# Optimization experiments

Hardware: AMD Instinct MI355X
Metric: run time of the kernel (lower is better)

Reference implementation:

```python
import jax, jax.numpy as jnp
import numpy as np

B, T, DIN, DOUT = 64, 512, 512, 512


def setup_inputs() -> dict:
    key = jax.random.key(0)
    ks = jax.random.split(key, 16)
    s = 0.05  # small scale ~ xavier/orthogonal magnitude
    inp = {
        "X": jax.random.normal(ks[0], (B, T, DIN), jnp.float32),
        "Wi": jax.random.normal(ks[1], (DOUT, DIN), jnp.float32) * s,
        "bi": jnp.zeros((DOUT,), jnp.float32),
        "Wf": jax.random.normal(ks[2], (DOUT, DIN), jnp.float32) * s,
        "bf": jnp.ones((DOUT,), jnp.float32),
        "Wc": jax.random.normal(ks[3], (DOUT, DIN), jnp.float32) * s,
        "bc": jnp.zeros((DOUT,), jnp.float32),
        "Wo": jax.random.normal(ks[4], (DOUT, DIN), jnp.float32) * s,
        "bo": jnp.zeros((DOUT,), jnp.float32),
        "Ui": jax.random.normal(ks[5], (DOUT, DOUT), jnp.float32) * s,
        "Uf": jax.random.normal(ks[6], (DOUT, DOUT), jnp.float32) * s,
        "bUf": jax.random.normal(ks[7], (DOUT,), jnp.float32) * s,
        "Uc": jax.random.normal(ks[8], (DOUT, DOUT), jnp.float32) * s,
        "bUc": jax.random.normal(ks[9], (DOUT,), jnp.float32) * s,
        "Uo": jax.random.normal(ks[10], (DOUT, DOUT), jnp.float32) * s,
        "bUo": jax.random.normal(ks[11], (DOUT,), jnp.float32) * s,
    }
    return inp


def reference(X, Wi, bi, Wf, bf, Wc, bc, Wo, bo, Ui, Uf, bUf, Uc, bUc, Uo, bUo):
    # Inference mode: dropout masks are ones, initial h/c are zeros.
    # Precompute input projections for all timesteps (as in the original).
    Xi = jnp.einsum('btd,od->bto', X, Wi) + bi  # [B,T,DOUT]
    Xf = jnp.einsum('btd,od->bto', X, Wf) + bf  # computed but UNUSED (faithful to source bug)
    Xc = jnp.einsum('btd,od->bto', X, Wc) + bc
    Xo = jnp.einsum('btd,od->bto', X, Wo) + bo

    h0 = jnp.zeros((X.shape[0], Wi.shape[0]), X.dtype)
    c0 = jnp.zeros_like(h0)

    def step(carry, xs):
        h, c = carry
        xi, xc, xo = xs
        i = jax.nn.sigmoid(xi + h @ Ui.T)                 # U_i has no bias
        f = jax.nn.sigmoid(xi + h @ Uf.T + bUf)           # NOTE: uses xi, not xf (source quirk)
        c_new = f * c + i * jnp.tanh(xc + h @ Uc.T + bUc)
        o = jax.nn.sigmoid(xo + h @ Uo.T + bUo)
        h_new = o * jnp.tanh(c_new)
        return (h_new, c_new), (h_new, c_new)

    xs = (Xi.transpose(1, 0, 2), Xc.transpose(1, 0, 2), Xo.transpose(1, 0, 2))  # [T,B,D]
    _, (H, C) = jax.lax.scan(step, (h0, c0), xs)
    return H.transpose(1, 0, 2), C.transpose(1, 0, 2)  # [B,T,DOUT] each
```

## Files before the change

### kernel.cpp

```cpp
#include <hip/hip_runtime.h>

#define B_    64
#define T_    512
#define D_    512
#define KF    1024
#define NGRP  4
#define NSLC  16
#define GB    16

using short8 = __attribute__((ext_vector_type(8))) short;
using f32x4  = __attribute__((ext_vector_type(4))) float;

__device__ __forceinline__ unsigned short f2bf(float f) {
    unsigned int u = __float_as_uint(f);
    u = (u + 0x7fffu + ((u >> 16) & 1u)) >> 16;
    return (unsigned short)u;
}
__device__ __forceinline__ float sigmf(float x)  { return 1.0f / (1.0f + __expf(-x)); }
__device__ __forceinline__ float tanh_f(float x) { return 1.0f - 2.0f / (1.0f + __expf(2.0f * x)); }

__global__ void prep_x(const float* __restrict__ X, unsigned short* __restrict__ Xb, int n4) {
    int stride = gridDim.x * blockDim.x;
    for (int i = blockIdx.x * blockDim.x + threadIdx.x; i < n4; i += stride) {
        float4 v = ((const float4*)X)[i];
        ushort4 o;
        o.x = f2bf(v.x); o.y = f2bf(v.y); o.z = f2bf(v.z); o.w = f2bf(v.w);
        ((ushort4*)Xb)[i] = o;
    }
}

__global__ void prep_w(const float* __restrict__ Wi, const float* __restrict__ Wc,
                       const float* __restrict__ Wo,
                       const float* __restrict__ Ui, const float* __restrict__ Uf,
                       const float* __restrict__ Uc, const float* __restrict__ Uo,
                       unsigned short* __restrict__ Wcat) {
    int idx = blockIdx.x * blockDim.x + threadIdx.x;
    if (idx >= 2048 * 1024) return;
    int r = idx >> 10, k = idx & 1023;
    int o = r >> 2, g = r & 3;
    const float* U = (g == 0) ? Ui : (g == 1) ? Uf : (g == 2) ? Uc : Uo;
    const float* W = (g < 2) ? Wi : (g == 2) ? Wc : Wo;
    float v = (k < 512) ? U[o * 512 + k] : W[o * 512 + (k - 512)];
    Wcat[idx] = f2bf(v);
}

__attribute__((amdgpu_waves_per_eu(2, 2)))
__launch_bounds__(512)
__global__ void lstm_rec(const unsigned short* __restrict__ Xb,
                         const unsigned short* __restrict__ Wcat,
                         unsigned short* __restrict__ hbuf,
                         unsigned int* __restrict__ hflag,
                         float* __restrict__ out,
                         const float* __restrict__ bi, const float* __restrict__ bc,
                         const float* __restrict__ bo, const float* __restrict__ bUf,
                         const float* __restrict__ bUc, const float* __restrict__ bUo) {
    __shared__ unsigned char Hl[16 * 1024];
    __shared__ unsigned char Xl[16 * 1024];

    const int tid  = threadIdx.x;
    const int bid  = blockIdx.x;
    const int g    = bid >> 4;
    const int s    = bid & 15;
    const int wave = tid >> 6;
    const int lane = tid & 63;
    const int q    = lane >> 4;
    const int bl   = lane & 15;

    const unsigned short* wrow = Wcat + (size_t)(s * 128 + wave * 16 + bl) * KF + q * 8;
    short8 Uh[16], Ux[16];
    #pragma unroll
    for (int kt = 0; kt < 16; ++kt) {
        union { unsigned long long u[2]; short8 v; } wh, wx;
        const unsigned long long* ph = (const unsigned long long*)(wrow + kt * 32);
        const unsigned long long* px = (const unsigned long long*)(wrow + 512 + kt * 32);
        wh.u[0] = __hip_atomic_load(ph,     __ATOMIC_RELAXED, __HIP_MEMORY_SCOPE_AGENT);
        wh.u[1] = __hip_atomic_load(ph + 1, __ATOMIC_RELAXED, __HIP_MEMORY_SCOPE_AGENT);
        wx.u[0] = __hip_atomic_load(px,     __ATOMIC_RELAXED, __HIP_MEMORY_SCOPE_AGENT);
        wx.u[1] = __hip_atomic_load(px + 1, __ATOMIC_RELAXED, __HIP_MEMORY_SCOPE_AGENT);
        Uh[kt] = wh.v;
        Ux[kt] = wx.v;
    }

    const int og = s * 32 + wave * 4 + q;
    const float bi0 = bi[og],           bf0 = bi[og] + bUf[og];
    const float bc0 = bc[og] + bUc[og], bo0 = bo[og] + bUo[og];
    float cst = 0.f;

    const int sb  = tid >> 5;
    const int seg = tid & 31;
    const int sx  = (sb & 7) << 4;
    unsigned int* pollp = hflag + (size_t)(g * NSLC + (seg >> 1)) * 16;
    unsigned int* myfl  = hflag + (size_t)(g * NSLC + s) * 16;
    const unsigned short* xst = Xb + (size_t)(g * GB + sb) * T_ * D_ + seg * 16;

    const unsigned short* xbl = Xb + (size_t)(g * GB + bl) * T_ * D_ + q * 8;
    const int abase = bl * 1024;
    const int axor  = (bl & 7) << 4;
    const int kq16  = q * 16;

    float* Hout = out;
    float* Cout = out + (size_t)B_ * T_ * D_;

    f32x4 xa0 = {0.f, 0.f, 0.f, 0.f}, xa1 = {0.f, 0.f, 0.f, 0.f};
    #pragma unroll
    for (int kt = 0; kt < 16; kt += 2) {
        short8 b0 = *(const short8*)(xbl + kt * 32);
        short8 b1 = *(const short8*)(xbl + (kt + 1) * 32);
        xa0 = __builtin_amdgcn_mfma_f32_16x16x32_bf16(Ux[kt],     b0, xa0, 0, 0, 0);
        xa1 = __builtin_amdgcn_mfma_f32_16x16x32_bf16(Ux[kt + 1], b1, xa1, 0, 0, 0);
    }

    for (int t = 0; t < T_; ++t) {
        uint4 xr0, xr1;
        const bool hasNext = (t + 1 < T_);
        if (hasNext) {
            const uint4* xs = (const uint4*)(xst + (size_t)(t + 1) * D_);
            xr0 = xs[0]; xr1 = xs[1];
        }

        f32x4 ha0 = {0.f, 0.f, 0.f, 0.f}, ha1 = {0.f, 0.f, 0.f, 0.f};
        if (t > 0) {
            while (__hip_atomic_load(pollp, __ATOMIC_RELAXED, __HIP_MEMORY_SCOPE_AGENT) < (unsigned)t) { }
            asm volatile("" ::: "memory");
            const unsigned long long* hs = (const unsigned long long*)
                (hbuf + ((size_t)((t + 1) & 1) * B_ + g * GB + sb) * D_ + seg * 16);
            unsigned long long d0 = __hip_atomic_load(hs + 0, __ATOMIC_RELAXED, __HIP_MEMORY_SCOPE_AGENT);
            unsigned long long d1 = __hip_atomic_load(hs + 1, __ATOMIC_RELAXED, __HIP_MEMORY_SCOPE_AGENT);
            unsigned long long d2 = __hip_atomic_load(hs + 2, __ATOMIC_RELAXED, __HIP_MEMORY_SCOPE_AGENT);
            unsigned long long d3 = __hip_atomic_load(hs + 3, __ATOMIC_RELAXED, __HIP_MEMORY_SCOPE_AGENT);
            *(uint4*)(Hl + sb * 1024 + ((seg * 32)      ^ sx)) =
                make_uint4((unsigned)d0, (unsigned)(d0 >> 32), (unsigned)d1, (unsigned)(d1 >> 32));
            *(uint4*)(Hl + sb * 1024 + ((seg * 32 + 16) ^ sx)) =
                make_uint4((unsigned)d2, (unsigned)(d2 >> 32), (unsigned)d3, (unsigned)(d3 >> 32));
            __syncthreads();
            #pragma unroll
            for (int kt = 0; kt < 16; kt += 2) {
                short8 a0 = *(const short8*)(Hl + abase + ((kq16 + kt * 64)       ^ axor));
                short8 a1 = *(const short8*)(Hl + abase + ((kq16 + (kt + 1) * 64) ^ axor));
                ha0 = __builtin_amdgcn_mfma_f32_16x16x32_bf16(Uh[kt],     a0, ha0, 0, 0, 0);
                ha1 = __builtin_amdgcn_mfma_f32_16x16x32_bf16(Uh[kt + 1], a1, ha1, 0, 0, 0);
            }
        }

        if (hasNext) {
            *(uint4*)(Xl + sb * 1024 + ((seg * 32)      ^ sx)) = xr0;
            *(uint4*)(Xl + sb * 1024 + ((seg * 32 + 16) ^ sx)) = xr1;
        }

        f32x4 A = (ha0 + ha1) + (xa0 + xa1);
        float iv = sigmf(A[0] + bi0);
        float fv = sigmf(A[1] + bf0);
        float cc = tanh_f(A[2] + bc0);
        float ov = sigmf(A[3] + bo0);
        float cv = fv * cst + iv * cc;
        float hv = ov * tanh_f(cv);
        cst = cv;

        __hip_atomic_store(hbuf + ((size_t)(t & 1) * B_ + g * GB + bl) * D_ + og,
                           f2bf(hv), __ATOMIC_RELAXED, __HIP_MEMORY_SCOPE_AGENT);
        __syncthreads();
        if (tid == 0)
            __hip_atomic_store(myfl, (unsigned)(t + 1), __ATOMIC_RELAXED, __HIP_MEMORY_SCOPE_AGENT);

        if (hasNext) {
            f32x4 n0 = {0.f, 0.f, 0.f, 0.f}, n1 = {0.f, 0.f, 0.f, 0.f};
            #pragma unroll
            for (int kt = 0; kt < 16; kt += 2) {
                short8 b0 = *(const short8*)(Xl + abase + ((kq16 + kt * 64)       ^ axor));
                short8 b1 = *(const short8*)(Xl + abase + ((kq16 + (kt + 1) * 64) ^ axor));
                n0 = __builtin_amdgcn_mfma_f32_16x16x32_bf16(Ux[kt],     b0, n0, 0, 0, 0);
                n1 = __builtin_amdgcn_mfma_f32_16x16x32_bf16(Ux[kt + 1], b1, n1, 0, 0, 0);
            }
            xa0 = n0; xa1 = n1;
        }

        const size_t oi = ((size_t)(g * GB + bl) * T_ + t) * D_ + og;
        Hout[oi] = hv;
        Cout[oi] = cv;
    }
}

extern "C" void kernel_launch(void* const* d_in, const int* in_sizes, int n_in,
                              void* d_out, int out_size, void* d_ws, size_t ws_size,
                              hipStream_t stream) {
    const float* X   = (const float*)d_in[0];
    const float* Wi  = (const float*)d_in[1];
    const float* bi  = (const float*)d_in[2];
    const float* Wc  = (const float*)d_in[5];
    const float* bc  = (const float*)d_in[6];
    const float* Wo  = (const float*)d_in[7];
    const float* bo  = (const float*)d_in[8];
    const float* Ui  = (const float*)d_in[9];
    const float* Uf  = (const float*)d_in[10];
    const float* bUf = (const float*)d_in[11];
    const float* Uc  = (const float*)d_in[12];
    const float* bUc = (const float*)d_in[13];
    const float* Uo  = (const float*)d_in[14];
    const float* bUo = (const float*)d_in[15];

    char* ws = (char*)d_ws;
    const size_t XB_BYTES   = (size_t)B_ * T_ * D_ * 2;
    const size_t WCAT_BYTES = (size_t)2048 * 1024 * 2;
    const size_t HBUF_BYTES = (size_t)2 * B_ * D_ * 2;
    const size_t FLAG_BYTES = (size_t)NGRP * NSLC * 16 * 4;

    unsigned short* Xb    = (unsigned short*)ws;
    unsigned short* Wcat  = (unsigned short*)(ws + XB_BYTES);
    unsigned short* hbuf  = (unsigned short*)(ws + XB_BYTES + WCAT_BYTES);
    unsigned int*   hflag = (unsigned int*)(ws + XB_BYTES + WCAT_BYTES + HBUF_BYTES);

    hipMemsetAsync(hbuf, 0, HBUF_BYTES + FLAG_BYTES, stream);

    prep_x<<<2048, 256, 0, stream>>>(X, Xb, B_ * T_ * D_ / 4);
    prep_w<<<8192, 256, 0, stream>>>(Wi, Wc, Wo, Ui, Uf, Uc, Uo, Wcat);
    lstm_rec<<<NGRP * NSLC, 512, 0, stream>>>(Xb, Wcat, hbuf, hflag, (float*)d_out,
                                              bi, bc, bo, bUf, bUc, bUo);
}
```

Baseline: 1.469 ms.

## Replace flag-based step sync with sequence-tagged h words and double buffers

Each h value is now stored as a 32-bit word that packs the bf16 value with the timestep number. Consumers poll the data words directly until every tag matches, which removes the separate flag store, the per-step barrier before it, and the extra flag round trip. X and H staging in shared memory is double-buffered and the X prefetch now runs two steps ahead. This leaves one barrier per step, and the next step's input projection is computed before the gate math. In exchange the h buffer doubles in size, and consumers spin on up to eight words per thread.

```diff
diff --git a/kernel.cpp b/kernel.cpp
--- a/kernel.cpp
+++ b/kernel.cpp
@@ -18,6 +18,16 @@
 }
 __device__ __forceinline__ float sigmf(float x)  { return 1.0f / (1.0f + __expf(-x)); }
 __device__ __forceinline__ float tanh_f(float x) { return 1.0f - 2.0f / (1.0f + __expf(2.0f * x)); }
+
+__device__ __forceinline__ int loff(int row, int kb) {
+    return row * 1024 + (kb ^ ((((row & 7) ^ ((kb >> 7) & 7)) << 4)));
+}
+__device__ __forceinline__ bool fresh2(unsigned long long w, unsigned want) {
+    return (((unsigned)w & 0xffffu) == want) & (((unsigned)(w >> 32) & 0xffffu) == want);
+}
+__device__ __forceinline__ unsigned pk(unsigned long long w) {
+    return (unsigned)((w >> 16) & 0xffffu) | ((unsigned)(w >> 32) & 0xffff0000u);
+}
 
 __global__ void prep_x(const float* __restrict__ X, unsigned short* __restrict__ Xb, int n4) {
     int stride = gridDim.x * blockDim.x;
@@ -44,18 +54,16 @@
     Wcat[idx] = f2bf(v);
 }
 
-__attribute__((amdgpu_waves_per_eu(2, 2)))
-__launch_bounds__(512)
+__launch_bounds__(512, 2)
 __global__ void lstm_rec(const unsigned short* __restrict__ Xb,
                          const unsigned short* __restrict__ Wcat,
-                         unsigned short* __restrict__ hbuf,
-                         unsigned int* __restrict__ hflag,
+                         unsigned int* __restrict__ hbuf,
                          float* __restrict__ out,
                          const float* __restrict__ bi, const float* __restrict__ bc,
                          const float* __restrict__ bo, const float* __restrict__ bUf,
                          const float* __restrict__ bUc, const float* __restrict__ bUo) {
-    __shared__ unsigned char Hl[16 * 1024];
-    __shared__ unsigned char Xl[16 * 1024];
+    __shared__ __align__(16) unsigned char Hl[2][16 * 1024];
+    __shared__ __align__(16) unsigned char Xl[2][16 * 1024];
 
     const int tid  = threadIdx.x;
     const int bid  = blockIdx.x;
@@ -88,15 +96,8 @@
 
     const int sb  = tid >> 5;
     const int seg = tid & 31;
-    const int sx  = (sb & 7) << 4;
-    unsigned int* pollp = hflag + (size_t)(g * NSLC + (seg >> 1)) * 16;
-    unsigned int* myfl  = hflag + (size_t)(g * NSLC + s) * 16;
     const unsigned short* xst = Xb + (size_t)(g * GB + sb) * T_ * D_ + seg * 16;
-
     const unsigned short* xbl = Xb + (size_t)(g * GB + bl) * T_ * D_ + q * 8;
-    const int abase = bl * 1024;
-    const int axor  = (bl & 7) << 4;
-    const int kq16  = q * 16;
 
     float* Hout = out;
     float* Cout = out + (size_t)B_ * T_ * D_;
@@ -109,42 +110,73 @@
         xa0 = __builtin_amdgcn_mfma_f32_16x16x32_bf16(Ux[kt],     b0, xa0, 0, 0, 0);
         xa1 = __builtin_amdgcn_mfma_f32_16x16x32_bf16(Ux[kt + 1], b1, xa1, 0, 0, 0);
     }
+    uint4 xc0, xc1;
+    {
+        const uint4* xs = (const uint4*)(xst + (size_t)1 * D_);
+        xc0 = xs[0]; xc1 = xs[1];
+    }
 
     for (int t = 0; t < T_; ++t) {
-        uint4 xr0, xr1;
+        const int cur = t & 1;
         const bool hasNext = (t + 1 < T_);
+
+        uint4 xn0v = xc0, xn1v = xc1;
+        if (t + 2 < T_) {
+            const uint4* xs = (const uint4*)(xst + (size_t)(t + 2) * D_);
+            xn0v = xs[0]; xn1v = xs[1];
+        }
+
+        if (t > 0) {
+            const unsigned long long* hw = (const unsigned long long*)
+                (hbuf + ((size_t)((t + 1) & 1) * B_ + g * GB + sb) * D_ + seg * 16);
+            const unsigned want = (unsigned)t;
+            unsigned long long w[8];
+            #pragma unroll
+            for (int k = 0; k < 8; ++k)
+                w[k] = __hip_atomic_load(hw + k, __ATOMIC_RELAXED, __HIP_MEMORY_SCOPE_AGENT);
+            bool again;
+            do {
+                again = false;
+                #pragma unroll
+                for (int k = 0; k < 8; ++k) {
+                    if (!fresh2(w[k], want)) {
+                        w[k] = __hip_atomic_load(hw + k, __ATOMIC_RELAXED, __HIP_MEMORY_SCOPE_AGENT);
+                        again = true;
+                    }
+                }
+            } while (again);
+            *(uint4*)(&Hl[cur][loff(sb, seg * 32)]) =
+                make_uint4(pk(w[0]), pk(w[1]), pk(w[2]), pk(w[3]));
+            *(uint4*)(&Hl[cur][loff(sb, seg * 32 + 16)]) =
+                make_uint4(pk(w[4]), pk(w[5]), pk(w[6]), pk(w[7]));
+        }
         if (hasNext) {
-            const uint4* xs = (const uint4*)(xst + (size_t)(t + 1) * D_);
-            xr0 = xs[0]; xr1 = xs[1];
-        }
+            *(uint4*)(&Xl[cur ^ 1][loff(sb, seg * 32)])      = xc0;
+            *(uint4*)(&Xl[cur ^ 1][loff(sb, seg * 32 + 16)]) = xc1;
+        }
+
+        asm volatile("s_waitcnt lgkmcnt(0)" ::: "memory");
+        __builtin_amdgcn_s_barrier();
 
         f32x4 ha0 = {0.f, 0.f, 0.f, 0.f}, ha1 = {0.f, 0.f, 0.f, 0.f};
         if (t > 0) {
-            while (__hip_atomic_load(pollp, __ATOMIC_RELAXED, __HIP_MEMORY_SCOPE_AGENT) < (unsigned)t) { }
-            asm volatile("" ::: "memory");
-            const unsigned long long* hs = (const unsigned long long*)
-                (hbuf + ((size_t)((t + 1) & 1) * B_ + g * GB + sb) * D_ + seg * 16);
-            unsigned long long d0 = __hip_atomic_load(hs + 0, __ATOMIC_RELAXED, __HIP_MEMORY_SCOPE_AGENT);
-            unsigned long long d1 = __hip_atomic_load(hs + 1, __ATOMIC_RELAXED, __HIP_MEMORY_SCOPE_AGENT);
-            unsigned long long d2 = __hip_atomic_load(hs + 2, __ATOMIC_RELAXED, __HIP_MEMORY_SCOPE_AGENT);
-            unsigned long long d3 = __hip_atomic_load(hs + 3, __ATOMIC_RELAXED, __HIP_MEMORY_SCOPE_AGENT);
-            *(uint4*)(Hl + sb * 1024 + ((seg * 32)      ^ sx)) =
-                make_uint4((unsigned)d0, (unsigned)(d0 >> 32), (unsigned)d1, (unsigned)(d1 >> 32));
-            *(uint4*)(Hl + sb * 1024 + ((seg * 32 + 16) ^ sx)) =
-                make_uint4((unsigned)d2, (unsigned)(d2 >> 32), (unsigned)d3, (unsigned)(d3 >> 32));
-            __syncthreads();
             #pragma unroll
             for (int kt = 0; kt < 16; kt += 2) {
-                short8 a0 = *(const short8*)(Hl + abase + ((kq16 + kt * 64)       ^ axor));
-                short8 a1 = *(const short8*)(Hl + abase + ((kq16 + (kt + 1) * 64) ^ axor));
+                short8 a0 = *(const short8*)(&Hl[cur][loff(bl, q * 16 + kt * 64)]);
+                short8 a1 = *(const short8*)(&Hl[cur][loff(bl, q * 16 + (kt + 1) * 64)]);
                 ha0 = __builtin_amdgcn_mfma_f32_16x16x32_bf16(Uh[kt],     a0, ha0, 0, 0, 0);
                 ha1 = __builtin_amdgcn_mfma_f32_16x16x32_bf16(Uh[kt + 1], a1, ha1, 0, 0, 0);
             }
         }
-
+        f32x4 xo0 = {0.f, 0.f, 0.f, 0.f}, xo1 = {0.f, 0.f, 0.f, 0.f};
         if (hasNext) {
-            *(uint4*)(Xl + sb * 1024 + ((seg * 32)      ^ sx)) = xr0;
-            *(uint4*)(Xl + sb * 1024 + ((seg * 32 + 16) ^ sx)) = xr1;
+            #pragma unroll
+            for (int kt = 0; kt < 16; kt += 2) {
+                short8 b0 = *(const short8*)(&Xl[cur ^ 1][loff(bl, q * 16 + kt * 64)]);
+                short8 b1 = *(const short8*)(&Xl[cur ^ 1][loff(bl, q * 16 + (kt + 1) * 64)]);
+                xo0 = __builtin_amdgcn_mfma_f32_16x16x32_bf16(Ux[kt],     b0, xo0, 0, 0, 0);
+                xo1 = __builtin_amdgcn_mfma_f32_16x16x32_bf16(Ux[kt + 1], b1, xo1, 0, 0, 0);
+            }
         }
 
         f32x4 A = (ha0 + ha1) + (xa0 + xa1);
@@ -155,28 +187,17 @@
         float cv = fv * cst + iv * cc;
         float hv = ov * tanh_f(cv);
         cst = cv;
-
-        __hip_atomic_store(hbuf + ((size_t)(t & 1) * B_ + g * GB + bl) * D_ + og,
-                           f2bf(hv), __ATOMIC_RELAXED, __HIP_MEMORY_SCOPE_AGENT);
-        __syncthreads();
-        if (tid == 0)
-            __hip_atomic_store(myfl, (unsigned)(t + 1), __ATOMIC_RELAXED, __HIP_MEMORY_SCOPE_AGENT);
-
-        if (hasNext) {
-            f32x4 n0 = {0.f, 0.f, 0.f, 0.f}, n1 = {0.f, 0.f, 0.f, 0.f};
-            #pragma unroll
-            for (int kt = 0; kt < 16; kt += 2) {
-                short8 b0 = *(const short8*)(Xl + abase + ((kq16 + kt * 64)       ^ axor));
-                short8 b1 = *(const short8*)(Xl + abase + ((kq16 + (kt + 1) * 64) ^ axor));
-                n0 = __builtin_amdgcn_mfma_f32_16x16x32_bf16(Ux[kt],     b0, n0, 0, 0, 0);
-                n1 = __builtin_amdgcn_mfma_f32_16x16x32_bf16(Ux[kt + 1], b1, n1, 0, 0, 0);
-            }
-            xa0 = n0; xa1 = n1;
-        }
+        xa0 = xo0; xa1 = xo1;
+
+        unsigned wrd = ((unsigned)f2bf(hv) << 16) | (unsigned)(t + 1);
+        __hip_atomic_store(hbuf + ((size_t)cur * B_ + g * GB + bl) * D_ + og,
+                           wrd, __ATOMIC_RELAXED, __HIP_MEMORY_SCOPE_AGENT);
 
         const size_t oi = ((size_t)(g * GB + bl) * T_ + t) * D_ + og;
         Hout[oi] = hv;
         Cout[oi] = cv;
+
+        xc0 = xn0v; xc1 = xn1v;
     }
 }
 
@@ -201,18 +222,16 @@
     char* ws = (char*)d_ws;
     const size_t XB_BYTES   = (size_t)B_ * T_ * D_ * 2;
     const size_t WCAT_BYTES = (size_t)2048 * 1024 * 2;
-    const size_t HBUF_BYTES = (size_t)2 * B_ * D_ * 2;
-    const size_t FLAG_BYTES = (size_t)NGRP * NSLC * 16 * 4;
-
-    unsigned short* Xb    = (unsigned short*)ws;
-    unsigned short* Wcat  = (unsigned short*)(ws + XB_BYTES);
-    unsigned short* hbuf  = (unsigned short*)(ws + XB_BYTES + WCAT_BYTES);
-    unsigned int*   hflag = (unsigned int*)(ws + XB_BYTES + WCAT_BYTES + HBUF_BYTES);
-
-    hipMemsetAsync(hbuf, 0, HBUF_BYTES + FLAG_BYTES, stream);
+    const size_t HBUF_BYTES = (size_t)2 * B_ * D_ * 4;
+
+    unsigned short* Xb   = (unsigned short*)ws;
+    unsigned short* Wcat = (unsigned short*)(ws + XB_BYTES);
+    unsigned int*   hbuf = (unsigned int*)(ws + XB_BYTES + WCAT_BYTES);
+
+    hipMemsetAsync(hbuf, 0, HBUF_BYTES, stream);
 
     prep_x<<<2048, 256, 0, stream>>>(X, Xb, B_ * T_ * D_ / 4);
     prep_w<<<8192, 256, 0, stream>>>(Wi, Wc, Wo, Ui, Uf, Uc, Uo, Wcat);
-    lstm_rec<<<NGRP * NSLC, 512, 0, stream>>>(Xb, Wcat, hbuf, hflag, (float*)d_out,
+    lstm_rec<<<NGRP * NSLC, 512, 0, stream>>>(Xb, Wcat, hbuf, (float*)d_out,
                                               bi, bc, bo, bUf, bUc, bUo);
 }
```

Result: slower. 3.800 ms (+158.7%).
